# Kernel tuning notes

Measured on AMD Instinct MI355X. Metric: run time of the kernel, lower is better.

Reference implementation:

```python
import jax, jax.numpy as jnp
import numpy as np

B = 64          # batch_size
H = 16384       # n_hidden
BS = 32         # block size of BlockSparseLinear
NB = H // BS    # 512 blocks per dim
NNZ = int(0.1 * NB * NB)  # 26214 nonzero blocks (density 0.1)
N_IN = 1024     # n_inputs
N_OUT = 1024    # n_outputs
STEPS = 8       # n_forward_steps


def setup_inputs() -> dict:
    key = jax.random.key(0)
    k1, k2, k3, k4, k5 = jax.random.split(key, 5)
    # kaiming-ish scale for effective fan-in = H * density
    w_scale = 1.0 / np.sqrt(H * 0.1)
    inp = jax.random.normal(k1, (B, N_IN), dtype=jnp.float32)
    blocks = jax.random.normal(k2, (NNZ, BS, BS), dtype=jnp.float32) * w_scale
    bias = jax.random.normal(k3, (H,), dtype=jnp.float32) * 0.01
    block_rows = jax.random.randint(k4, (NNZ,), 0, NB, dtype=jnp.int32)
    block_cols = jax.random.randint(k5, (NNZ,), 0, NB, dtype=jnp.int32)
    return {"inp": inp, "blocks": blocks, "bias": bias,
            "block_rows": block_rows, "block_cols": block_cols}


def _block_sparse_linear(blocks, block_rows, block_cols, bias, x):
    # x: [B, H] -> y = W_sparse @ x + bias, W stored as NNZ 32x32 blocks
    xb = x.reshape(B, NB, BS)[:, block_cols]               # [B, NNZ, BS]
    contrib = jnp.einsum('nij,bnj->nbi', blocks, xb)       # [NNZ, B, BS]
    yb = jax.ops.segment_sum(contrib, block_rows, num_segments=NB)  # [NB, B, BS]
    return yb.transpose(1, 0, 2).reshape(B, H) + bias


def reference(inp, blocks, bias, block_rows, block_cols):
    # hs = zeros[B, H]; first n_inputs slots get the input (squeeze trailing 1-dim)
    hs = jnp.zeros((B, H), dtype=inp.dtype).at[:, :N_IN].set(inp)
    for step in range(STEPS):
        hs = _block_sparse_linear(blocks, block_rows, block_cols, bias, hs)
        if step != STEPS - 1:
            hs = jax.nn.sigmoid(hs)
    # output_act = sigmoid on last n_outputs entries
    return jax.nn.sigmoid(hs[:, -N_OUT:])
```

## Files before the change

### kernel.cpp

```cpp
#include <hip/hip_runtime.h>
#include <stdint.h>

#define B_     64
#define H_     16384
#define NB_    512
#define NNZ_   26214
#define N_IN_  1024
#define N_OUT_ 1024

typedef __attribute__((ext_vector_type(8))) short    bf16x8;
typedef __attribute__((ext_vector_type(4))) float    f32x4;
typedef __attribute__((ext_vector_type(4))) unsigned int u32x4;

__device__ __forceinline__ unsigned short f2bf(float f) {
    union { unsigned int i; float f; } v; v.f = f;
    unsigned int x = v.i;
    return (unsigned short)((x + 0x7fffu + ((x >> 16) & 1u)) >> 16);
}

__device__ __forceinline__ bf16x8 ldfrag(const unsigned short* p) {
    union { u32x4 u; bf16x8 b; } cv;
    cv.u = *(const u32x4*)p;
    return cv.b;
}

__device__ __forceinline__ bf16x8 ldfrag_nt(const unsigned short* p) {
    union { u32x4 u; bf16x8 b; } cv;
    cv.u = __builtin_nontemporal_load((const u32x4*)p);
    return cv.b;
}


__global__ void zero_cnt(int* __restrict__ cnt) { cnt[threadIdx.x] = 0; }

__global__ void hist(const int* __restrict__ rows, int* __restrict__ cnt) {
    int n = blockIdx.x * 256 + threadIdx.x;
    if (n < NNZ_) atomicAdd(&cnt[rows[n]], 1);
}

__global__ void scan_k(int* __restrict__ cnt, int* __restrict__ ptr) {
    __shared__ int tmp[NB_];
    int t = threadIdx.x;
    tmp[t] = cnt[t];
    __syncthreads();
    for (int off = 1; off < NB_; off <<= 1) {
        int v = (t >= off) ? tmp[t - off] : 0;
        __syncthreads();
        tmp[t] += v;
        __syncthreads();
    }
    if (t == 0) ptr[0] = 0;
    ptr[t + 1] = tmp[t];
    cnt[t] = 0;
}

__global__ void scatter2(const int* __restrict__ rows, const int* __restrict__ cols,
                         const int* __restrict__ ptr, int* __restrict__ cnt,
                         int2* __restrict__ pair2) {
    int n = blockIdx.x * 256 + threadIdx.x;
    if (n < NNZ_) {
        int r = rows[n];
        int pos = ptr[r] + atomicAdd(&cnt[r], 1);
        pair2[pos] = make_int2(n, cols[n]);
    }
}


__global__ __launch_bounds__(256) void conv_w(const float* __restrict__ w,
                                              unsigned short* __restrict__ wb,
                                              const int2* __restrict__ pair2) {
    int pos = blockIdx.x;
    int t   = threadIdx.x;
    int n   = pair2[pos].x;
    f32x4 v = __builtin_nontemporal_load((const f32x4*)(w + (size_t)n * 1024) + t);
    union { unsigned short s[4]; uint2 d; } o;
    o.s[0] = f2bf(v[0]); o.s[1] = f2bf(v[1]); o.s[2] = f2bf(v[2]); o.s[3] = f2bf(v[3]);
    ((uint2*)(wb + (size_t)pos * 1024))[t] = o.d;
}


__global__ __launch_bounds__(256) void init_x(const float* __restrict__ inp,
                                              unsigned short* __restrict__ xb) {
    int idx = blockIdx.x * 256 + threadIdx.x;
    int c = idx >> 11;
    int b = (idx >> 5) & 63;
    int j = idx & 31;
    int h = c * 32 + j;
    xb[idx] = (h < N_IN_) ? f2bf(inp[b * N_IN_ + h]) : (unsigned short)0;
}

#define MFMA8(A, Bv)                                                         \
    do {                                                                     \
        _Pragma("unroll")                                                    \
        for (int mt = 0; mt < 2; ++mt)                                       \
            _Pragma("unroll")                                                \
            for (int nt = 0; nt < 4; ++nt)                                   \
                acc[mt][nt] = __builtin_amdgcn_mfma_f32_16x16x32_bf16(       \
                                  A[mt], Bv[nt], acc[mt][nt], 0, 0, 0);      \
    } while (0)

template <bool LAST>
__global__ __launch_bounds__(512, 4) void rowstep_k(
        const unsigned short* __restrict__ x,
        unsigned short* __restrict__ xout,
        float* __restrict__ out,
        const unsigned short* __restrict__ wb,
        const float* __restrict__ bias,
        const int2* __restrict__ pair2,
        const int* __restrict__ ptr,
        int row_base, int col_limit) {
    __shared__ int2  s_pairs[8][64];
    __shared__ float s_red[8][64][33];

    const int r    = blockIdx.x + row_base;
    const int tid  = threadIdx.x;
    const int wv   = tid >> 6;
    const int lane = tid & 63;
    const int half = lane & 15;
    const int quad = lane >> 4;

    const int beg = ptr[r], cnt = ptr[r + 1] - beg;
    const int c0 = beg + (cnt * wv) / 8;
    const int m  = beg + (cnt * (wv + 1)) / 8 - c0;

    int2 pc = make_int2(0, 0);
    bool valid = (lane < m);
    if (valid) {
        int c = pair2[c0 + lane].y;
        pc = make_int2(c0 + lane, c);
        valid = (c < col_limit);
    }
    unsigned long long mask = __ballot(valid);
    if (valid) {
        int pos = __popcll(mask & ((1ull << lane) - 1ull));
        s_pairs[wv][pos] = pc;
    }
    const int mv = __popcll(mask);

    f32x4 acc[2][4] = {};

    bf16x8 A0[2], B0[4], A1[2], B1[4];
    #define LDFRAGS(A, Bv, p)                                                  \
        do {                                                                   \
            const unsigned short* wp =                                         \
                wb + (size_t)(p).x * 1024 + half * 32 + quad * 8;              \
            A[0] = ldfrag_nt(wp);                                              \
            A[1] = ldfrag_nt(wp + 16 * 32);                                    \
            const unsigned short* xp =                                         \
                x + ((size_t)(p).y * 64 + half) * 32 + quad * 8;               \
            Bv[0] = ldfrag(xp);                                                \
            Bv[1] = ldfrag(xp + 16 * 32);                                      \
            Bv[2] = ldfrag(xp + 32 * 32);                                      \
            Bv[3] = ldfrag(xp + 48 * 32);                                      \
        } while (0)

    if (mv > 0) { int2 p = s_pairs[wv][0]; LDFRAGS(A0, B0, p); }
    int j = 0;
    while (j + 2 <= mv) {
        { int2 p = s_pairs[wv][j + 1]; LDFRAGS(A1, B1, p); }
        MFMA8(A0, B0);
        if (j + 2 < mv) { int2 p = s_pairs[wv][j + 2]; LDFRAGS(A0, B0, p); }
        MFMA8(A1, B1);
        j += 2;
    }
    if (j < mv) MFMA8(A0, B0);

    #pragma unroll
    for (int mt = 0; mt < 2; ++mt)
        #pragma unroll
        for (int nt = 0; nt < 4; ++nt)
            #pragma unroll
            for (int q2 = 0; q2 < 4; ++q2)
                s_red[wv][nt * 16 + half][mt * 16 + quad * 4 + q2] = acc[mt][nt][q2];
    __syncthreads();

    const int b  = tid >> 3;
    const int i0 = (tid & 7) * 4;
    const float4 bv = *(const float4*)&bias[r * 32 + i0];
    float v[4] = {bv.x, bv.y, bv.z, bv.w};
    #pragma unroll
    for (int w = 0; w < 8; ++w)
        #pragma unroll
        for (int k = 0; k < 4; ++k)
            v[k] += s_red[w][b][i0 + k];
    if (LAST) {
        float4 o;
        o.x = 1.0f / (1.0f + __expf(-v[0]));
        o.y = 1.0f / (1.0f + __expf(-v[1]));
        o.z = 1.0f / (1.0f + __expf(-v[2]));
        o.w = 1.0f / (1.0f + __expf(-v[3]));
        *(float4*)&out[(size_t)b * N_OUT_ + (r - (NB_ - N_OUT_ / 32)) * 32 + i0] = o;
    } else {
        union { unsigned short s[4]; uint2 u; } o;
        #pragma unroll
        for (int k = 0; k < 4; ++k)
            o.s[k] = f2bf(1.0f / (1.0f + __expf(-v[k])));
        *(uint2*)&xout[((size_t)r * 64 + b) * 32 + i0] = o.u;
    }
}


extern "C" void kernel_launch(void* const* d_in, const int* in_sizes, int n_in,
                              void* d_out, int out_size, void* d_ws, size_t ws_size,
                              hipStream_t stream) {
    const float* inp    = (const float*)d_in[0];
    const float* blocks = (const float*)d_in[1];
    const float* bias   = (const float*)d_in[2];
    const int*   rows   = (const int*)d_in[3];
    const int*   cols   = (const int*)d_in[4];
    float*       out    = (float*)d_out;

    char* ws = (char*)d_ws;
    unsigned short* wbf = (unsigned short*)ws;
    unsigned short* x0  = (unsigned short*)(ws + 53686272u);
    unsigned short* x1  = (unsigned short*)(ws + 53686272u + 2097152u);
    char*  idxbase      = ws + 53686272u + 2u * 2097152u;
    int*   rowptr = (int*)(idxbase);
    int*   rowcnt = (int*)(idxbase + 4096);
    int2*  pair2  = (int2*)(idxbase + 8192);

    zero_cnt<<<1, NB_, 0, stream>>>(rowcnt);
    hist<<<(NNZ_ + 255) / 256, 256, 0, stream>>>(rows, rowcnt);
    scan_k<<<1, NB_, 0, stream>>>(rowcnt, rowptr);
    scatter2<<<(NNZ_ + 255) / 256, 256, 0, stream>>>(rows, cols, rowptr, rowcnt, pair2);

    conv_w<<<NNZ_, 256, 0, stream>>>(blocks, wbf, pair2);

    init_x<<<(B_ * H_) / 256, 256, 0, stream>>>(inp, x0);

    unsigned short* cur = x0;
    unsigned short* nxt = x1;
    rowstep_k<false><<<NB_, 512, 0, stream>>>(cur, nxt, nullptr, wbf, bias,
                                              pair2, rowptr, 0, 32);
    { unsigned short* t = cur; cur = nxt; nxt = t; }
    for (int s = 1; s < 7; ++s) {
        rowstep_k<false><<<NB_, 512, 0, stream>>>(cur, nxt, nullptr, wbf, bias,
                                                  pair2, rowptr, 0, NB_);
        unsigned short* t = cur; cur = nxt; nxt = t;
    }
    rowstep_k<true><<<N_OUT_ / 32, 512, 0, stream>>>(cur, nullptr, out, wbf, bias,
                                                     pair2, rowptr,
                                                     NB_ - N_OUT_ / 32, NB_);
}
```

Baseline: 318.7 us.

## Fuse all eight forward steps into one cooperative kernel with grid sync

Replaces the eight per-step rowstep launches with a single cooperative kernel that loops over steps and uses grid.sync between them. Each block keeps its row's pair list and bias in registers across steps. Shared-memory reduction is halved (two-stage add into 4 slots), which may raise occupancy. Weight loads switch from nontemporal to normal loads so the bf16 weights can stay cached across steps. It adds grid-wide barrier cost and needs all 512 blocks co-resident, and it falls back to the old launches if the cooperative launch fails.

```diff
diff --git a/kernel.cpp b/kernel.cpp
--- a/kernel.cpp
+++ b/kernel.cpp
@@ -1,5 +1,8 @@
 #include <hip/hip_runtime.h>
+#include <hip/hip_cooperative_groups.h>
 #include <stdint.h>
+
+namespace cg = cooperative_groups;
 
 #define B_     64
 #define H_     16384
@@ -21,12 +24,6 @@
 __device__ __forceinline__ bf16x8 ldfrag(const unsigned short* p) {
     union { u32x4 u; bf16x8 b; } cv;
     cv.u = *(const u32x4*)p;
-    return cv.b;
-}
-
-__device__ __forceinline__ bf16x8 ldfrag_nt(const unsigned short* p) {
-    union { u32x4 u; bf16x8 b; } cv;
-    cv.u = __builtin_nontemporal_load((const u32x4*)p);
     return cv.b;
 }
 
@@ -89,6 +86,7 @@
     xb[idx] = (h < N_IN_) ? f2bf(inp[b * N_IN_ + h]) : (unsigned short)0;
 }
 
+
 #define MFMA8(A, Bv)                                                         \
     do {                                                                     \
         _Pragma("unroll")                                                    \
@@ -98,6 +96,132 @@
                 acc[mt][nt] = __builtin_amdgcn_mfma_f32_16x16x32_bf16(       \
                                   A[mt], Bv[nt], acc[mt][nt], 0, 0, 0);      \
     } while (0)
+
+#define LDFRAGS(A, Bv, p)                                                    \
+    do {                                                                     \
+        const unsigned short* wp =                                           \
+            wb + (size_t)(p).x * 1024 + half * 32 + quad * 8;                \
+        A[0] = ldfrag(wp);                                                   \
+        A[1] = ldfrag(wp + 16 * 32);                                         \
+        const unsigned short* xp =                                           \
+            x + ((size_t)(p).y * 64 + half) * 32 + quad * 8;                 \
+        Bv[0] = ldfrag(xp);                                                  \
+        Bv[1] = ldfrag(xp + 16 * 32);                                        \
+        Bv[2] = ldfrag(xp + 32 * 32);                                        \
+        Bv[3] = ldfrag(xp + 48 * 32);                                        \
+    } while (0)
+
+
+__global__ __launch_bounds__(512, 4) void fused_k(
+        const unsigned short* __restrict__ xa,
+        unsigned short* __restrict__ xb_,
+        float* __restrict__ out,
+        const unsigned short* __restrict__ wb,
+        const float* __restrict__ bias,
+        const int2* __restrict__ pair2,
+        const int* __restrict__ ptr) {
+    __shared__ int2  s_pairs[8][64];
+    __shared__ float s_red[4][64][33];
+
+    const int r    = blockIdx.x;
+    const int tid  = threadIdx.x;
+    const int wv   = tid >> 6;
+    const int lane = tid & 63;
+    const int half = lane & 15;
+    const int quad = lane >> 4;
+
+    const int beg = ptr[r], cnt = ptr[r + 1] - beg;
+    const int c0 = beg + (cnt * wv) / 8;
+    const int m  = beg + (cnt * (wv + 1)) / 8 - c0;
+
+    int2 pcl = make_int2(0, 0);
+    const bool have = (lane < m);
+    if (have) pcl = make_int2(c0 + lane, pair2[c0 + lane].y);
+
+    const int b  = tid >> 3;
+    const int i0 = (tid & 7) * 4;
+    const float4 bv = *(const float4*)&bias[r * 32 + i0];
+
+    cg::grid_group grid = cg::this_grid();
+
+    for (int step = 0; step < 8; ++step) {
+        const bool last = (step == 7);
+        if (!last || r >= NB_ - N_OUT_ / 32) {
+            const unsigned short* x  = (step & 1) ? xb_ : xa;
+            unsigned short*       xo = (step & 1) ? const_cast<unsigned short*>(xa) : xb_;
+            const int col_limit = (step == 0) ? (N_IN_ / 32) : NB_;
+
+            bool valid = have && (pcl.y < col_limit);
+            unsigned long long mask = __ballot(valid);
+            if (valid) {
+                int pos = __popcll(mask & ((1ull << lane) - 1ull));
+                s_pairs[wv][pos] = pcl;
+            }
+            const int mv = __popcll(mask);
+
+            f32x4 acc[2][4] = {};
+            bf16x8 A0[2], B0[4], A1[2], B1[4];
+
+            if (mv > 0) { int2 p = s_pairs[wv][0]; LDFRAGS(A0, B0, p); }
+            int j = 0;
+            while (j + 2 <= mv) {
+                { int2 p = s_pairs[wv][j + 1]; LDFRAGS(A1, B1, p); }
+                MFMA8(A0, B0);
+                if (j + 2 < mv) { int2 p = s_pairs[wv][j + 2]; LDFRAGS(A0, B0, p); }
+                MFMA8(A1, B1);
+                j += 2;
+            }
+            if (j < mv) MFMA8(A0, B0);
+
+            if (wv >= 4) {
+                #pragma unroll
+                for (int mt = 0; mt < 2; ++mt)
+                    #pragma unroll
+                    for (int nt = 0; nt < 4; ++nt)
+                        #pragma unroll
+                        for (int q2 = 0; q2 < 4; ++q2)
+                            s_red[wv - 4][nt * 16 + half][mt * 16 + quad * 4 + q2] =
+                                acc[mt][nt][q2];
+            }
+            __syncthreads();
+            if (wv < 4) {
+                #pragma unroll
+                for (int mt = 0; mt < 2; ++mt)
+                    #pragma unroll
+                    for (int nt = 0; nt < 4; ++nt)
+                        #pragma unroll
+                        for (int q2 = 0; q2 < 4; ++q2)
+                            s_red[wv][nt * 16 + half][mt * 16 + quad * 4 + q2] +=
+                                acc[mt][nt][q2];
+            }
+            __syncthreads();
+
+            float v[4] = {bv.x, bv.y, bv.z, bv.w};
+            #pragma unroll
+            for (int w = 0; w < 4; ++w)
+                #pragma unroll
+                for (int k = 0; k < 4; ++k)
+                    v[k] += s_red[w][b][i0 + k];
+            if (last) {
+                float4 o;
+                o.x = 1.0f / (1.0f + __expf(-v[0]));
+                o.y = 1.0f / (1.0f + __expf(-v[1]));
+                o.z = 1.0f / (1.0f + __expf(-v[2]));
+                o.w = 1.0f / (1.0f + __expf(-v[3]));
+                *(float4*)&out[(size_t)b * N_OUT_ +
+                               (r - (NB_ - N_OUT_ / 32)) * 32 + i0] = o;
+            } else {
+                union { unsigned short s[4]; uint2 u; } o;
+                #pragma unroll
+                for (int k = 0; k < 4; ++k)
+                    o.s[k] = f2bf(1.0f / (1.0f + __expf(-v[k])));
+                *(uint2*)&xo[((size_t)r * 64 + b) * 32 + i0] = o.u;
+            }
+        }
+        if (step < 7) grid.sync();
+    }
+}
+
 
 template <bool LAST>
 __global__ __launch_bounds__(512, 4) void rowstep_k(
@@ -110,7 +234,7 @@
         const int* __restrict__ ptr,
         int row_base, int col_limit) {
     __shared__ int2  s_pairs[8][64];
-    __shared__ float s_red[8][64][33];
+    __shared__ float s_red[4][64][33];
 
     const int r    = blockIdx.x + row_base;
     const int tid  = threadIdx.x;
@@ -138,21 +262,7 @@
     const int mv = __popcll(mask);
 
     f32x4 acc[2][4] = {};
-
     bf16x8 A0[2], B0[4], A1[2], B1[4];
-    #define LDFRAGS(A, Bv, p)                                                  \
-        do {                                                                   \
-            const unsigned short* wp =                                         \
-                wb + (size_t)(p).x * 1024 + half * 32 + quad * 8;              \
-            A[0] = ldfrag_nt(wp);                                              \
-            A[1] = ldfrag_nt(wp + 16 * 32);                                    \
-            const unsigned short* xp =                                         \
-                x + ((size_t)(p).y * 64 + half) * 32 + quad * 8;               \
-            Bv[0] = ldfrag(xp);                                                \
-            Bv[1] = ldfrag(xp + 16 * 32);                                      \
-            Bv[2] = ldfrag(xp + 32 * 32);                                      \
-            Bv[3] = ldfrag(xp + 48 * 32);                                      \
-        } while (0)
 
     if (mv > 0) { int2 p = s_pairs[wv][0]; LDFRAGS(A0, B0, p); }
     int j = 0;
@@ -165,13 +275,27 @@
     }
     if (j < mv) MFMA8(A0, B0);
 
-    #pragma unroll
-    for (int mt = 0; mt < 2; ++mt)
+    if (wv >= 4) {
         #pragma unroll
-        for (int nt = 0; nt < 4; ++nt)
+        for (int mt = 0; mt < 2; ++mt)
             #pragma unroll
-            for (int q2 = 0; q2 < 4; ++q2)
-                s_red[wv][nt * 16 + half][mt * 16 + quad * 4 + q2] = acc[mt][nt][q2];
+            for (int nt = 0; nt < 4; ++nt)
+                #pragma unroll
+                for (int q2 = 0; q2 < 4; ++q2)
+                    s_red[wv - 4][nt * 16 + half][mt * 16 + quad * 4 + q2] =
+                        acc[mt][nt][q2];
+    }
+    __syncthreads();
+    if (wv < 4) {
+        #pragma unroll
+        for (int mt = 0; mt < 2; ++mt)
+            #pragma unroll
+            for (int nt = 0; nt < 4; ++nt)
+                #pragma unroll
+                for (int q2 = 0; q2 < 4; ++q2)
+                    s_red[wv][nt * 16 + half][mt * 16 + quad * 4 + q2] +=
+                        acc[mt][nt][q2];
+    }
     __syncthreads();
 
     const int b  = tid >> 3;
@@ -179,7 +303,7 @@
     const float4 bv = *(const float4*)&bias[r * 32 + i0];
     float v[4] = {bv.x, bv.y, bv.z, bv.w};
     #pragma unroll
-    for (int w = 0; w < 8; ++w)
+    for (int w = 0; w < 4; ++w)
         #pragma unroll
         for (int k = 0; k < 4; ++k)
             v[k] += s_red[w][b][i0 + k];
@@ -228,17 +352,25 @@
 
     init_x<<<(B_ * H_) / 256, 256, 0, stream>>>(inp, x0);
 
-    unsigned short* cur = x0;
-    unsigned short* nxt = x1;
-    rowstep_k<false><<<NB_, 512, 0, stream>>>(cur, nxt, nullptr, wbf, bias,
-                                              pair2, rowptr, 0, 32);
-    { unsigned short* t = cur; cur = nxt; nxt = t; }
-    for (int s = 1; s < 7; ++s) {
+    void* kargs[] = { (void*)&x0, (void*)&x1, (void*)&out, (void*)&wbf,
+                      (void*)&bias, (void*)&pair2, (void*)&rowptr };
+    hipError_t ce = hipLaunchCooperativeKernel(
+        reinterpret_cast<void*>(fused_k), dim3(NB_), dim3(512), kargs, 0, stream);
+
+    if (ce != hipSuccess) {
+        (void)hipGetLastError();
+        unsigned short* cur = x0;
+        unsigned short* nxt = x1;
         rowstep_k<false><<<NB_, 512, 0, stream>>>(cur, nxt, nullptr, wbf, bias,
-                                                  pair2, rowptr, 0, NB_);
-        unsigned short* t = cur; cur = nxt; nxt = t;
-    }
-    rowstep_k<true><<<N_OUT_ / 32, 512, 0, stream>>>(cur, nullptr, out, wbf, bias,
-                                                     pair2, rowptr,
-                                                     NB_ - N_OUT_ / 32, NB_);
-}
+                                                  pair2, rowptr, 0, 32);
+        { unsigned short* t = cur; cur = nxt; nxt = t; }
+        for (int s = 1; s < 7; ++s) {
+            rowstep_k<false><<<NB_, 512, 0, stream>>>(cur, nxt, nullptr, wbf, bias,
+                                                      pair2, rowptr, 0, NB_);
+            unsigned short* t = cur; cur = nxt; nxt = t;
+        }
+        rowstep_k<true><<<N_OUT_ / 32, 512, 0, stream>>>(cur, nullptr, out, wbf, bias,
+                                                         pair2, rowptr,
+                                                         NB_ - N_OUT_ / 32, NB_);
+    }
+}
```

Result: slower. 716.7 us (+124.9%).

## Split first step kernel, triple-buffer fragment loads, halve reduction LDS

Applied to the files above, without the earlier changes.

The generic row-step kernel is split in two. A specialized first-step kernel keeps the column filter, and a full-row kernel drops the ballot/LDS pair list, broadcasting each x offset with readlane and walking the row's sorted weight blocks contiguously. The full kernel uses a three-stage register prefetch instead of two to hide more load latency. The cross-wave reduction now stages only 4 waves in LDS and accumulates the other 4 in place, halving shared memory and the epilogue reads at the cost of an extra barrier. Nontemporal loads on weights are replaced with normal loads, and the extra fragment registers may raise register pressure.

```diff
diff --git a/kernel.cpp b/kernel.cpp
--- a/kernel.cpp
+++ b/kernel.cpp
@@ -21,12 +21,6 @@
 __device__ __forceinline__ bf16x8 ldfrag(const unsigned short* p) {
     union { u32x4 u; bf16x8 b; } cv;
     cv.u = *(const u32x4*)p;
-    return cv.b;
-}
-
-__device__ __forceinline__ bf16x8 ldfrag_nt(const unsigned short* p) {
-    union { u32x4 u; bf16x8 b; } cv;
-    cv.u = __builtin_nontemporal_load((const u32x4*)p);
     return cv.b;
 }
 
@@ -89,6 +83,7 @@
     xb[idx] = (h < N_IN_) ? f2bf(inp[b * N_IN_ + h]) : (unsigned short)0;
 }
 
+
 #define MFMA8(A, Bv)                                                         \
     do {                                                                     \
         _Pragma("unroll")                                                    \
@@ -99,8 +94,59 @@
                                   A[mt], Bv[nt], acc[mt][nt], 0, 0, 0);      \
     } while (0)
 
+#define REDUCE_EPILOGUE(LASTF)                                               \
+    do {                                                                     \
+        if (wv >= 4) {                                                       \
+            _Pragma("unroll")                                                \
+            for (int mt = 0; mt < 2; ++mt)                                   \
+                _Pragma("unroll")                                            \
+                for (int nt = 0; nt < 4; ++nt)                               \
+                    _Pragma("unroll")                                        \
+                    for (int q2 = 0; q2 < 4; ++q2)                           \
+                        s_red[wv - 4][nt * 16 + half][mt * 16 + quad * 4 + q2] = \
+                            acc[mt][nt][q2];                                 \
+        }                                                                    \
+        __syncthreads();                                                     \
+        if (wv < 4) {                                                        \
+            _Pragma("unroll")                                                \
+            for (int mt = 0; mt < 2; ++mt)                                   \
+                _Pragma("unroll")                                            \
+                for (int nt = 0; nt < 4; ++nt)                               \
+                    _Pragma("unroll")                                        \
+                    for (int q2 = 0; q2 < 4; ++q2)                           \
+                        s_red[wv][nt * 16 + half][mt * 16 + quad * 4 + q2] += \
+                            acc[mt][nt][q2];                                 \
+        }                                                                    \
+        __syncthreads();                                                     \
+        const int b  = tid >> 3;                                             \
+        const int i0 = (tid & 7) * 4;                                        \
+        const float4 bv = *(const float4*)&bias[r * 32 + i0];                \
+        float v[4] = {bv.x, bv.y, bv.z, bv.w};                               \
+        _Pragma("unroll")                                                    \
+        for (int w = 0; w < 4; ++w)                                          \
+            _Pragma("unroll")                                                \
+            for (int k = 0; k < 4; ++k)                                      \
+                v[k] += s_red[w][b][i0 + k];                                 \
+        if (LASTF) {                                                         \
+            float4 o;                                                        \
+            o.x = 1.0f / (1.0f + __expf(-v[0]));                             \
+            o.y = 1.0f / (1.0f + __expf(-v[1]));                             \
+            o.z = 1.0f / (1.0f + __expf(-v[2]));                             \
+            o.w = 1.0f / (1.0f + __expf(-v[3]));                             \
+            *(float4*)&out[(size_t)b * N_OUT_ +                              \
+                           (r - (NB_ - N_OUT_ / 32)) * 32 + i0] = o;         \
+        } else {                                                             \
+            union { unsigned short s[4]; uint2 u; } o;                       \
+            _Pragma("unroll")                                                \
+            for (int k = 0; k < 4; ++k)                                      \
+                o.s[k] = f2bf(1.0f / (1.0f + __expf(-v[k])));                \
+            *(uint2*)&xout[((size_t)r * 64 + b) * 32 + i0] = o.u;            \
+        }                                                                    \
+    } while (0)
+
+
 template <bool LAST>
-__global__ __launch_bounds__(512, 4) void rowstep_k(
+__global__ __launch_bounds__(512, 4) void rowfull_k(
         const unsigned short* __restrict__ x,
         unsigned short* __restrict__ xout,
         float* __restrict__ out,
@@ -108,9 +154,8 @@
         const float* __restrict__ bias,
         const int2* __restrict__ pair2,
         const int* __restrict__ ptr,
-        int row_base, int col_limit) {
-    __shared__ int2  s_pairs[8][64];
-    __shared__ float s_red[8][64][33];
+        int row_base) {
+    __shared__ float s_red[4][64][33];
 
     const int r    = blockIdx.x + row_base;
     const int tid  = threadIdx.x;
@@ -120,6 +165,72 @@
     const int quad = lane >> 4;
 
     const int beg = ptr[r], cnt = ptr[r + 1] - beg;
+    const int c0 = __builtin_amdgcn_readfirstlane(beg + (cnt * wv) / 8);
+    const int mv = __builtin_amdgcn_readfirstlane(beg + (cnt * (wv + 1)) / 8 - c0);
+
+    int xoff = 0;
+    if (lane < mv) xoff = pair2[c0 + lane].y * 2048;
+
+    const int off16 = half * 32 + quad * 8;
+    const unsigned short* wbase = wb + (size_t)c0 * 1024 + off16;
+
+    f32x4 acc[2][4] = {};
+    bf16x8 A0[2], B0[4], A1[2], B1[4], A2[2], B2[4];
+
+    #define LDST(A, Bv, t)                                                   \
+        do {                                                                 \
+            int tt = ((t) < mv - 1) ? (t) : (mv - 1);                        \
+            const unsigned short* wp = wbase + (size_t)tt * 1024;            \
+            A[0] = ldfrag(wp);                                               \
+            A[1] = ldfrag(wp + 512);                                         \
+            int xo = __builtin_amdgcn_readlane(xoff, tt);                    \
+            const unsigned short* xp = x + xo + off16;                       \
+            Bv[0] = ldfrag(xp);                                              \
+            Bv[1] = ldfrag(xp + 512);                                        \
+            Bv[2] = ldfrag(xp + 1024);                                       \
+            Bv[3] = ldfrag(xp + 1536);                                       \
+        } while (0)
+
+    if (mv > 0) {
+        LDST(A0, B0, 0);
+        LDST(A1, B1, 1);
+        LDST(A2, B2, 2);
+        int j = 0;
+        while (j + 3 < mv) {
+            MFMA8(A0, B0); LDST(A0, B0, j + 3);
+            MFMA8(A1, B1); LDST(A1, B1, j + 4);
+            MFMA8(A2, B2); LDST(A2, B2, j + 5);
+            j += 3;
+        }
+        MFMA8(A0, B0);
+        if (mv - j > 1) MFMA8(A1, B1);
+        if (mv - j > 2) MFMA8(A2, B2);
+    }
+    #undef LDST
+
+    REDUCE_EPILOGUE(LAST);
+}
+
+
+__global__ __launch_bounds__(512, 4) void rowstep0_k(
+        const unsigned short* __restrict__ x,
+        unsigned short* __restrict__ xout,
+        const unsigned short* __restrict__ wb,
+        const float* __restrict__ bias,
+        const int2* __restrict__ pair2,
+        const int* __restrict__ ptr) {
+    __shared__ int2  s_pairs[8][64];
+    __shared__ float s_red[4][64][33];
+    float* __restrict__ out = nullptr;
+
+    const int r    = blockIdx.x;
+    const int tid  = threadIdx.x;
+    const int wv   = tid >> 6;
+    const int lane = tid & 63;
+    const int half = lane & 15;
+    const int quad = lane >> 4;
+
+    const int beg = ptr[r], cnt = ptr[r + 1] - beg;
     const int c0 = beg + (cnt * wv) / 8;
     const int m  = beg + (cnt * (wv + 1)) / 8 - c0;
 
@@ -128,7 +239,7 @@
     if (valid) {
         int c = pair2[c0 + lane].y;
         pc = make_int2(c0 + lane, c);
-        valid = (c < col_limit);
+        valid = (c < N_IN_ / 32);
     }
     unsigned long long mask = __ballot(valid);
     if (valid) {
@@ -137,66 +248,36 @@
     }
     const int mv = __popcll(mask);
 
+    const int off16 = half * 32 + quad * 8;
+
     f32x4 acc[2][4] = {};
-
     bf16x8 A0[2], B0[4], A1[2], B1[4];
-    #define LDFRAGS(A, Bv, p)                                                  \
-        do {                                                                   \
-            const unsigned short* wp =                                         \
-                wb + (size_t)(p).x * 1024 + half * 32 + quad * 8;              \
-            A[0] = ldfrag_nt(wp);                                              \
-            A[1] = ldfrag_nt(wp + 16 * 32);                                    \
-            const unsigned short* xp =                                         \
-                x + ((size_t)(p).y * 64 + half) * 32 + quad * 8;               \
-            Bv[0] = ldfrag(xp);                                                \
-            Bv[1] = ldfrag(xp + 16 * 32);                                      \
-            Bv[2] = ldfrag(xp + 32 * 32);                                      \
-            Bv[3] = ldfrag(xp + 48 * 32);                                      \
+
+    #define LDFRAGS0(A, Bv, p)                                               \
+        do {                                                                 \
+            const unsigned short* wp = wb + (size_t)(p).x * 1024 + off16;    \
+            A[0] = ldfrag(wp);                                               \
+            A[1] = ldfrag(wp + 512);                                         \
+            const unsigned short* xp = x + (size_t)(p).y * 2048 + off16;     \
+            Bv[0] = ldfrag(xp);                                              \
+            Bv[1] = ldfrag(xp + 512);                                        \
+            Bv[2] = ldfrag(xp + 1024);                                       \
+            Bv[3] = ldfrag(xp + 1536);                                       \
         } while (0)
 
-    if (mv > 0) { int2 p = s_pairs[wv][0]; LDFRAGS(A0, B0, p); }
+    if (mv > 0) { int2 p = s_pairs[wv][0]; LDFRAGS0(A0, B0, p); }
     int j = 0;
     while (j + 2 <= mv) {
-        { int2 p = s_pairs[wv][j + 1]; LDFRAGS(A1, B1, p); }
+        { int2 p = s_pairs[wv][j + 1]; LDFRAGS0(A1, B1, p); }
         MFMA8(A0, B0);
-        if (j + 2 < mv) { int2 p = s_pairs[wv][j + 2]; LDFRAGS(A0, B0, p); }
+        if (j + 2 < mv) { int2 p = s_pairs[wv][j + 2]; LDFRAGS0(A0, B0, p); }
         MFMA8(A1, B1);
         j += 2;
     }
     if (j < mv) MFMA8(A0, B0);
-
-    #pragma unroll
-    for (int mt = 0; mt < 2; ++mt)
-        #pragma unroll
-        for (int nt = 0; nt < 4; ++nt)
-            #pragma unroll
-            for (int q2 = 0; q2 < 4; ++q2)
-                s_red[wv][nt * 16 + half][mt * 16 + quad * 4 + q2] = acc[mt][nt][q2];
-    __syncthreads();
-
-    const int b  = tid >> 3;
-    const int i0 = (tid & 7) * 4;
-    const float4 bv = *(const float4*)&bias[r * 32 + i0];
-    float v[4] = {bv.x, bv.y, bv.z, bv.w};
-    #pragma unroll
-    for (int w = 0; w < 8; ++w)
-        #pragma unroll
-        for (int k = 0; k < 4; ++k)
-            v[k] += s_red[w][b][i0 + k];
-    if (LAST) {
-        float4 o;
-        o.x = 1.0f / (1.0f + __expf(-v[0]));
-        o.y = 1.0f / (1.0f + __expf(-v[1]));
-        o.z = 1.0f / (1.0f + __expf(-v[2]));
-        o.w = 1.0f / (1.0f + __expf(-v[3]));
-        *(float4*)&out[(size_t)b * N_OUT_ + (r - (NB_ - N_OUT_ / 32)) * 32 + i0] = o;
-    } else {
-        union { unsigned short s[4]; uint2 u; } o;
-        #pragma unroll
-        for (int k = 0; k < 4; ++k)
-            o.s[k] = f2bf(1.0f / (1.0f + __expf(-v[k])));
-        *(uint2*)&xout[((size_t)r * 64 + b) * 32 + i0] = o.u;
-    }
+    #undef LDFRAGS0
+
+    REDUCE_EPILOGUE(false);
 }
 
 
@@ -230,15 +311,14 @@
 
     unsigned short* cur = x0;
     unsigned short* nxt = x1;
-    rowstep_k<false><<<NB_, 512, 0, stream>>>(cur, nxt, nullptr, wbf, bias,
-                                              pair2, rowptr, 0, 32);
+    rowstep0_k<<<NB_, 512, 0, stream>>>(cur, nxt, wbf, bias, pair2, rowptr);
     { unsigned short* t = cur; cur = nxt; nxt = t; }
     for (int s = 1; s < 7; ++s) {
-        rowstep_k<false><<<NB_, 512, 0, stream>>>(cur, nxt, nullptr, wbf, bias,
-                                                  pair2, rowptr, 0, NB_);
+        rowfull_k<false><<<NB_, 512, 0, stream>>>(cur, nxt, nullptr, wbf, bias,
+                                                  pair2, rowptr, 0);
         unsigned short* t = cur; cur = nxt; nxt = t;
     }
-    rowstep_k<true><<<N_OUT_ / 32, 512, 0, stream>>>(cur, nullptr, out, wbf, bias,
+    rowfull_k<true><<<N_OUT_ / 32, 512, 0, stream>>>(cur, nullptr, out, wbf, bias,
                                                      pair2, rowptr,
-                                                     NB_ - N_OUT_ / 32, NB_);
-}
+                                                     NB_ - N_OUT_ / 32);
+}
```

Measured after the change: 311.4 us. -2.3%, faster.
